# Kernel optimization log

Hardware: AMD Instinct MI355X
Metric: run time of the kernel (lower is better)

The kernel has to match this reference:

```python
import jax, jax.numpy as jnp
import numpy as np

T, B, D = 512, 64, 1024


def setup_inputs() -> dict:
    key = jax.random.key(0)
    k1, k2, k3, k4, k5 = jax.random.split(key, 5)
    s = 1.0 / np.sqrt(D)  # torch RNNCell init scale
    return {
        "x": jax.random.normal(k1, (T, B, D), dtype=jnp.float32),
        "W_ih": jax.random.normal(k2, (D, D), dtype=jnp.float32) * s,
        "W_hh": jax.random.normal(k3, (D, D), dtype=jnp.float32) * s,
        "b_ih": jax.random.normal(k4, (D,), dtype=jnp.float32) * s,
        "b_hh": jax.random.normal(k5, (D,), dtype=jnp.float32) * s,
    }


def reference(x, W_ih, W_hh, b_ih, b_hh):
    """CustomRNN forward: sequential Elman cell over time-major input.

    x: [T, B, D]; returns (output [T, B, D], final hidden [B, D]).
    """
    # Precompute the input projection for all timesteps in one big GEMM
    # (same math as per-step x_t @ W_ih^T + b_ih, just batched).
    xproj = jnp.einsum("tbd,hd->tbh", x, W_ih) + b_ih  # [T, B, D]

    def step(h, xp_t):
        h_new = jnp.tanh(xp_t + h @ W_hh.T + b_hh)  # [B, D]
        return h_new, h_new

    h0 = jnp.zeros((x.shape[1], W_hh.shape[0]), dtype=x.dtype)
    h_final, output = jax.lax.scan(step, h0, xproj)
    return output, h_final
```

## Files before the change

kernel.cpp:

```cpp
#include <hip/hip_runtime.h>
#include <hip/hip_bf16.h>

#define T_LEN 512
#define B_SZ  64
#define D_SZ  1024

typedef __attribute__((ext_vector_type(8))) short  short8;
typedef __attribute__((ext_vector_type(4))) float  f32x4;
typedef __attribute__((ext_vector_type(4))) unsigned short ushort4v;
typedef __attribute__((ext_vector_type(4))) unsigned int   uint4v;

__device__ __forceinline__ float bf2f(unsigned short u) {
    unsigned int x = ((unsigned int)u) << 16;
    return __uint_as_float(x);
}
__device__ __forceinline__ unsigned short f2bf(float f) {
    unsigned int x = __float_as_uint(f);
    unsigned int r = x + 0x7FFFu + ((x >> 16) & 1u);
    return (unsigned short)(r >> 16);
}
__device__ __forceinline__ void split2p(float f, unsigned short* hi, unsigned short* lo) {
    unsigned short h = f2bf(f);
    *hi = h;
    *lo = f2bf(f - bf2f(h));
}

#define CNT_STRIDE 64

__global__ void init_kernel(int* slot) {
    int i = threadIdx.x;
    if (i < 8 * CNT_STRIDE) slot[i] = 0;
}

#define BM 128
#define BN 128
#define BK 32
#define ASTR (BK + 8)

__global__ __launch_bounds__(256) void xproj_kernel(
    const float* __restrict__ x, const float* __restrict__ Wih,
    const float* __restrict__ bih, float* __restrict__ xp)
{
    __shared__ unsigned short Ah[BM][ASTR];
    __shared__ unsigned short Al[BM][ASTR];
    __shared__ unsigned short Bh[BN][ASTR];
    __shared__ unsigned short Bl[BN][ASTR];

    const int nblk = D_SZ / BN;
    const int bm = blockIdx.x / nblk;
    const int bn = blockIdx.x % nblk;
    const int m0 = bm * BM, n0 = bn * BN;
    const int tid  = threadIdx.x;
    const int lane = tid & 63, wave = tid >> 6;
    const int wm = wave >> 1, wn = wave & 1;

    f32x4 acc[4][4];
#pragma unroll
    for (int i = 0; i < 4; i++)
#pragma unroll
        for (int j = 0; j < 4; j++) acc[i][j] = (f32x4)0.0f;

    const int ar = lane & 15;
    const int kb = (lane >> 4) << 3;

    for (int k0 = 0; k0 < D_SZ; k0 += BK) {
#pragma unroll
        for (int i = 0; i < 4; i++) {
            int f4  = tid + i * 256;
            int row = f4 >> 3;
            int c4  = (f4 & 7) << 2;
            f32x4 va = *reinterpret_cast<const f32x4*>(x   + (size_t)(m0 + row) * D_SZ + k0 + c4);
            f32x4 vb = *reinterpret_cast<const f32x4*>(Wih + (size_t)(n0 + row) * D_SZ + k0 + c4);
            ushort4v pah, pal, pbh, pbl;
#pragma unroll
            for (int e = 0; e < 4; e++) {
                unsigned short h_, l_;
                split2p(va[e], &h_, &l_); pah[e] = h_; pal[e] = l_;
                split2p(vb[e], &h_, &l_); pbh[e] = h_; pbl[e] = l_;
            }
            *reinterpret_cast<ushort4v*>(&Ah[row][c4]) = pah;
            *reinterpret_cast<ushort4v*>(&Al[row][c4]) = pal;
            *reinterpret_cast<ushort4v*>(&Bh[row][c4]) = pbh;
            *reinterpret_cast<ushort4v*>(&Bl[row][c4]) = pbl;
        }
        __syncthreads();

        short8 ah[4], al[4], bh[4], bl[4];
#pragma unroll
        for (int mi = 0; mi < 4; mi++) {
            ah[mi] = *reinterpret_cast<const short8*>(&Ah[wm * 64 + mi * 16 + ar][kb]);
            al[mi] = *reinterpret_cast<const short8*>(&Al[wm * 64 + mi * 16 + ar][kb]);
        }
#pragma unroll
        for (int ni = 0; ni < 4; ni++) {
            bh[ni] = *reinterpret_cast<const short8*>(&Bh[wn * 64 + ni * 16 + ar][kb]);
            bl[ni] = *reinterpret_cast<const short8*>(&Bl[wn * 64 + ni * 16 + ar][kb]);
        }
#pragma unroll
        for (int mi = 0; mi < 4; mi++)
#pragma unroll
            for (int ni = 0; ni < 4; ni++) {
                acc[mi][ni] = __builtin_amdgcn_mfma_f32_16x16x32_bf16(ah[mi], bh[ni], acc[mi][ni], 0, 0, 0);
                acc[mi][ni] = __builtin_amdgcn_mfma_f32_16x16x32_bf16(al[mi], bh[ni], acc[mi][ni], 0, 0, 0);
                acc[mi][ni] = __builtin_amdgcn_mfma_f32_16x16x32_bf16(ah[mi], bl[ni], acc[mi][ni], 0, 0, 0);
            }
        __syncthreads();
    }

    const int r0 = (lane >> 4) * 4;
    const int cl = lane & 15;
#pragma unroll
    for (int mi = 0; mi < 4; mi++) {
#pragma unroll
        for (int ni = 0; ni < 4; ni++) {
            int col = n0 + wn * 64 + ni * 16 + cl;
            float bias = bih[col];
            size_t base = (size_t)(m0 + wm * 64 + mi * 16 + r0) * D_SZ + col;
#pragma unroll
            for (int r = 0; r < 4; r++)
                xp[base + (size_t)r * D_SZ] = acc[mi][ni][r] + bias;
        }
    }
}

#define MR 8
#define NC 32
#define HSTR (D_SZ + 8)

__global__ __launch_bounds__(128, 1) void rnn_kernel(
    const float* __restrict__ xp, const float* __restrict__ Whh,
    const float* __restrict__ bhh, float* __restrict__ out,
    unsigned int* hbuf, int* slot)
{
    __shared__ unsigned short Hh[16][HSTR];
    __shared__ unsigned short Hl[16][HSTR];
    __shared__ unsigned short Wlo[2][16][HSTR];

    const int wg = blockIdx.x;
    const int b  = wg & 7;
    const int c  = wg >> 3;
    const int tid  = threadIdx.x;
    const int lane = tid & 63, wave = tid >> 6;

    const int cl   = lane & 15;
    const int hi4  = lane >> 4;
    const int kb   = hi4 << 3;
    const int colg = c * NC + wave * 16 + cl;
    const float bias = bhh[colg];
    const int rloc = hi4 * 4;
    const bool active = (hi4 < 2);

    int* tslot = slot + b * CNT_STRIDE;
    const int myslot = c * 2 + wave;

    short8 wh[32];
    {
        const float* wrow = Whh + (size_t)colg * D_SZ;
#pragma unroll
        for (int kk = 0; kk < 32; kk++) {
            f32x4 v0 = *reinterpret_cast<const f32x4*>(wrow + kk * 32 + kb);
            f32x4 v1 = *reinterpret_cast<const f32x4*>(wrow + kk * 32 + kb + 4);
            short8 sh, sl;
#pragma unroll
            for (int e = 0; e < 4; e++) {
                unsigned short h_, l_;
                split2p(v0[e], &h_, &l_); sh[e] = (short)h_; sl[e] = (short)l_;
                split2p(v1[e], &h_, &l_); sh[4 + e] = (short)h_; sl[4 + e] = (short)l_;
            }
            wh[kk] = sh;
            *reinterpret_cast<short8*>(&Wlo[wave][cl][kk * 32 + kb]) = sl;
        }
    }
    for (int i = tid; i < 16 * HSTR; i += 128) {
        (&Hh[0][0])[i] = 0;
        (&Hl[0][0])[i] = 0;
    }
    __syncthreads();

    for (int t = 0; t < T_LEN; t++) {
        float xv[4];
        const float* xpt = xp + ((size_t)t * B_SZ + b * MR) * D_SZ;
        if (active) {
#pragma unroll
            for (int r = 0; r < 4; r++)
                xv[r] = xpt[(size_t)(rloc + r) * D_SZ + colg];
        }

        if (t > 0) {
            for (int tries = 0; tries < 400000; ++tries) {
                int v = __hip_atomic_load(tslot + lane, __ATOMIC_RELAXED, __HIP_MEMORY_SCOPE_AGENT);
                if (__all(v >= t)) break;
            }

            const uint4v* hsrc16 = reinterpret_cast<const uint4v*>(
                hbuf + ((size_t)(t & 1) * B_SZ + b * MR) * D_SZ);
            uint4v vv[16];
#pragma unroll
            for (int i = 0; i < 16; i++)
                asm volatile("global_load_dwordx4 %0, %1, off sc0 sc1"
                             : "=v"(vv[i]) : "v"(hsrc16 + tid + i * 128) : "memory");
            asm volatile("s_waitcnt vmcnt(8)" ::: "memory");
            __builtin_amdgcn_sched_barrier(0);
#pragma unroll
            for (int i = 0; i < 8; i++) {
                int j   = tid + i * 128;
                int row = j >> 8;
                int c4  = (j & 255) << 2;
                ushort4v hh, hl;
#pragma unroll
                for (int e = 0; e < 4; e++) {
                    unsigned int u = vv[i][e];
                    hh[e] = (unsigned short)(u & 0xFFFFu);
                    hl[e] = (unsigned short)(u >> 16);
                }
                *reinterpret_cast<ushort4v*>(&Hh[row][c4]) = hh;
                *reinterpret_cast<ushort4v*>(&Hl[row][c4]) = hl;
            }
            asm volatile("s_waitcnt vmcnt(0)" ::: "memory");
            __builtin_amdgcn_sched_barrier(0);
#pragma unroll
            for (int i = 8; i < 16; i++) {
                int j   = tid + i * 128;
                int row = j >> 8;
                int c4  = (j & 255) << 2;
                ushort4v hh, hl;
#pragma unroll
                for (int e = 0; e < 4; e++) {
                    unsigned int u = vv[i][e];
                    hh[e] = (unsigned short)(u & 0xFFFFu);
                    hl[e] = (unsigned short)(u >> 16);
                }
                *reinterpret_cast<ushort4v*>(&Hh[row][c4]) = hh;
                *reinterpret_cast<ushort4v*>(&Hl[row][c4]) = hl;
            }
            __syncthreads();
        }

        f32x4 a0 = (f32x4)0.0f, a1 = (f32x4)0.0f, a2 = (f32x4)0.0f;
#pragma unroll
        for (int kk = 0; kk < 32; kk++) {
            short8 ah  = *reinterpret_cast<const short8*>(&Hh[cl][kk * 32 + kb]);
            short8 alo = *reinterpret_cast<const short8*>(&Hl[cl][kk * 32 + kb]);
            short8 wlv = *reinterpret_cast<const short8*>(&Wlo[wave][cl][kk * 32 + kb]);
            a0 = __builtin_amdgcn_mfma_f32_16x16x32_bf16(ah,  wh[kk], a0, 0, 0, 0);
            a1 = __builtin_amdgcn_mfma_f32_16x16x32_bf16(alo, wh[kk], a1, 0, 0, 0);
            a2 = __builtin_amdgcn_mfma_f32_16x16x32_bf16(ah,  wlv,    a2, 0, 0, 0);
        }

        float hval[4];
        if (active) {
            unsigned int* hdst = hbuf + ((size_t)((t + 1) & 1) * B_SZ + b * MR) * D_SZ;
#pragma unroll
            for (int r = 0; r < 4; r++) {
                int row = rloc + r;
                float pre = (a0[r] + a1[r] + a2[r]) + xv[r] + bias;
                float h = tanhf(pre);
                hval[r] = h;
                unsigned short hh_, ll_;
                split2p(h, &hh_, &ll_);
                unsigned int packed = (unsigned int)hh_ | ((unsigned int)ll_ << 16);
                __hip_atomic_store(&hdst[(size_t)row * D_SZ + colg], packed,
                                   __ATOMIC_RELAXED, __HIP_MEMORY_SCOPE_AGENT);
            }
        }
        asm volatile("s_waitcnt vmcnt(0)" ::: "memory");
        if (lane == 0)
            __hip_atomic_store(tslot + myslot, t + 1, __ATOMIC_RELAXED, __HIP_MEMORY_SCOPE_AGENT);

        if (active) {
            float* outt = out + ((size_t)t * B_SZ + b * MR) * D_SZ;
#pragma unroll
            for (int r = 0; r < 4; r++) {
                int row = rloc + r;
                outt[(size_t)row * D_SZ + colg] = hval[r];
                if (t == T_LEN - 1)
                    out[(size_t)T_LEN * B_SZ * D_SZ + (size_t)(b * MR + row) * D_SZ + colg] = hval[r];
            }
        }
    }
}

extern "C" void kernel_launch(void* const* d_in, const int* in_sizes, int n_in,
                              void* d_out, int out_size, void* d_ws, size_t ws_size,
                              hipStream_t stream)
{
    const float* x   = (const float*)d_in[0];
    const float* Wih = (const float*)d_in[1];
    const float* Whh = (const float*)d_in[2];
    const float* bih = (const float*)d_in[3];
    const float* bhh = (const float*)d_in[4];
    float* out = (float*)d_out;

    char* ws = (char*)d_ws;
    float*        xp   = (float*)ws;
    unsigned int* hbuf = (unsigned int*)(ws + 134217728);
    int*          slot = (int*)(ws + 134217728 + 524288);

    init_kernel<<<dim3(1), dim3(512), 0, stream>>>(slot);
    xproj_kernel<<<dim3(2048), dim3(256), 0, stream>>>(x, Wih, bih, xp);
    rnn_kernel<<<dim3(256), dim3(128), 0, stream>>>(xp, Whh, bhh, out, hbuf, slot);
}
```

Measured before the change: 2.307 ms.

## Overlap second half of hidden-state load with first-half MFMAs, keep half of W_lo in registers

The hidden-state loads are reordered so the first batch covers the columns needed by the first 16 K-steps. The MFMAs for that half run while the second batch of loads is still in flight, and the second half is unpacked afterwards. Half of the W low-part fragments move from LDS into registers, which shrinks LDS traffic but raises register pressure. tanhf is replaced by an exp-based fast tanh, which is cheaper but slightly less accurate.

```diff
diff --git a/kernel.cpp b/kernel.cpp
--- a/kernel.cpp
+++ b/kernel.cpp
@@ -23,6 +23,11 @@
     unsigned short h = f2bf(f);
     *hi = h;
     *lo = f2bf(f - bf2f(h));
+}
+__device__ __forceinline__ float fast_tanh(float x) {
+    float xx = fminf(fmaxf(x, -20.0f), 20.0f);
+    float e2 = __expf(2.0f * xx);
+    return __fdividef(e2 - 1.0f, e2 + 1.0f);
 }
 
 #define CNT_STRIDE 64
@@ -126,6 +131,7 @@
 #define MR 8
 #define NC 32
 #define HSTR (D_SZ + 8)
+#define WSTR 520
 
 __global__ __launch_bounds__(128, 1) void rnn_kernel(
     const float* __restrict__ xp, const float* __restrict__ Whh,
@@ -134,7 +140,7 @@
 {
     __shared__ unsigned short Hh[16][HSTR];
     __shared__ unsigned short Hl[16][HSTR];
-    __shared__ unsigned short Wlo[2][16][HSTR];
+    __shared__ unsigned short Wlo[2][16][WSTR];
 
     const int wg = blockIdx.x;
     const int b  = wg & 7;
@@ -153,7 +159,7 @@
     int* tslot = slot + b * CNT_STRIDE;
     const int myslot = c * 2 + wave;
 
-    short8 wh[32];
+    short8 wh[32], wl_r[16];
     {
         const float* wrow = Whh + (size_t)colg * D_SZ;
 #pragma unroll
@@ -168,7 +174,8 @@
                 split2p(v1[e], &h_, &l_); sh[4 + e] = (short)h_; sl[4 + e] = (short)l_;
             }
             wh[kk] = sh;
-            *reinterpret_cast<short8*>(&Wlo[wave][cl][kk * 32 + kb]) = sl;
+            if (kk < 16) wl_r[kk] = sl;
+            else *reinterpret_cast<short8*>(&Wlo[wave][cl][(kk - 16) * 32 + kb]) = sl;
         }
     }
     for (int i = tid; i < 16 * HSTR; i += 128) {
@@ -186,47 +193,65 @@
                 xv[r] = xpt[(size_t)(rloc + r) * D_SZ + colg];
         }
 
+        uint4v vv[16];
         if (t > 0) {
             for (int tries = 0; tries < 400000; ++tries) {
                 int v = __hip_atomic_load(tslot + lane, __ATOMIC_RELAXED, __HIP_MEMORY_SCOPE_AGENT);
                 if (__all(v >= t)) break;
             }
 
+            asm volatile("s_waitcnt vmcnt(0)" ::: "memory");
+
             const uint4v* hsrc16 = reinterpret_cast<const uint4v*>(
                 hbuf + ((size_t)(t & 1) * B_SZ + b * MR) * D_SZ);
-            uint4v vv[16];
-#pragma unroll
-            for (int i = 0; i < 16; i++)
+#pragma unroll
+            for (int s = 0; s < 16; s++) {
+                int i = (s < 8) ? (2 * s) : (2 * (s - 8) + 1);
                 asm volatile("global_load_dwordx4 %0, %1, off sc0 sc1"
-                             : "=v"(vv[i]) : "v"(hsrc16 + tid + i * 128) : "memory");
+                             : "=v"(vv[s]) : "v"(hsrc16 + tid + i * 128) : "memory");
+            }
             asm volatile("s_waitcnt vmcnt(8)" ::: "memory");
             __builtin_amdgcn_sched_barrier(0);
 #pragma unroll
-            for (int i = 0; i < 8; i++) {
-                int j   = tid + i * 128;
+            for (int s = 0; s < 8; s++) {
+                int j   = tid + (2 * s) * 128;
                 int row = j >> 8;
                 int c4  = (j & 255) << 2;
                 ushort4v hh, hl;
 #pragma unroll
                 for (int e = 0; e < 4; e++) {
-                    unsigned int u = vv[i][e];
+                    unsigned int u = vv[s][e];
                     hh[e] = (unsigned short)(u & 0xFFFFu);
                     hl[e] = (unsigned short)(u >> 16);
                 }
                 *reinterpret_cast<ushort4v*>(&Hh[row][c4]) = hh;
                 *reinterpret_cast<ushort4v*>(&Hl[row][c4]) = hl;
             }
+            __syncthreads();
+        }
+
+        f32x4 a0 = (f32x4)0.0f, a1 = (f32x4)0.0f, a2 = (f32x4)0.0f;
+#pragma unroll
+        for (int kk = 0; kk < 16; kk++) {
+            short8 ah  = *reinterpret_cast<const short8*>(&Hh[cl][kk * 32 + kb]);
+            short8 alo = *reinterpret_cast<const short8*>(&Hl[cl][kk * 32 + kb]);
+            a0 = __builtin_amdgcn_mfma_f32_16x16x32_bf16(ah,  wh[kk],   a0, 0, 0, 0);
+            a1 = __builtin_amdgcn_mfma_f32_16x16x32_bf16(alo, wh[kk],   a1, 0, 0, 0);
+            a2 = __builtin_amdgcn_mfma_f32_16x16x32_bf16(ah,  wl_r[kk], a2, 0, 0, 0);
+        }
+
+        if (t > 0) {
             asm volatile("s_waitcnt vmcnt(0)" ::: "memory");
             __builtin_amdgcn_sched_barrier(0);
 #pragma unroll
-            for (int i = 8; i < 16; i++) {
-                int j   = tid + i * 128;
+            for (int s = 8; s < 16; s++) {
+                int j   = tid + (2 * (s - 8) + 1) * 128;
                 int row = j >> 8;
                 int c4  = (j & 255) << 2;
                 ushort4v hh, hl;
 #pragma unroll
                 for (int e = 0; e < 4; e++) {
-                    unsigned int u = vv[i][e];
+                    unsigned int u = vv[s][e];
                     hh[e] = (unsigned short)(u & 0xFFFFu);
                     hl[e] = (unsigned short)(u >> 16);
                 }
@@ -236,12 +261,11 @@
             __syncthreads();
         }
 
-        f32x4 a0 = (f32x4)0.0f, a1 = (f32x4)0.0f, a2 = (f32x4)0.0f;
-#pragma unroll
-        for (int kk = 0; kk < 32; kk++) {
+#pragma unroll
+        for (int kk = 16; kk < 32; kk++) {
             short8 ah  = *reinterpret_cast<const short8*>(&Hh[cl][kk * 32 + kb]);
             short8 alo = *reinterpret_cast<const short8*>(&Hl[cl][kk * 32 + kb]);
-            short8 wlv = *reinterpret_cast<const short8*>(&Wlo[wave][cl][kk * 32 + kb]);
+            short8 wlv = *reinterpret_cast<const short8*>(&Wlo[wave][cl][(kk - 16) * 32 + kb]);
             a0 = __builtin_amdgcn_mfma_f32_16x16x32_bf16(ah,  wh[kk], a0, 0, 0, 0);
             a1 = __builtin_amdgcn_mfma_f32_16x16x32_bf16(alo, wh[kk], a1, 0, 0, 0);
             a2 = __builtin_amdgcn_mfma_f32_16x16x32_bf16(ah,  wlv,    a2, 0, 0, 0);
@@ -254,7 +278,7 @@
             for (int r = 0; r < 4; r++) {
                 int row = rloc + r;
                 float pre = (a0[r] + a1[r] + a2[r]) + xv[r] + bias;
-                float h = tanhf(pre);
+                float h = fast_tanh(pre);
                 hval[r] = h;
                 unsigned short hh_, ll_;
                 split2p(h, &hh_, &ll_);
```

New measurement: 2.475 ms. 1.07x slower.
